# Kernel optimization log

Hardware: AMD Instinct MI355X
Metric: run time of the kernel (lower is better)

Reference implementation:

```python
import jax, jax.numpy as jnp
import numpy as np

EPS = 1e-15
BALL_EPS = 1e-5  # geoopt-style clamp away from the ball boundary


def expmap0(u):
    # Poincare ball (curvature -1): expmap0(u) = tanh(||u||) * u / ||u||
    n = jnp.linalg.norm(u, axis=-1, keepdims=True)
    n = jnp.maximum(n, EPS)
    return jnp.tanh(n) * u / n


def setup_inputs() -> dict:
    key = jax.random.key(0)
    k1, k2, k3 = jax.random.split(key, 3)
    B, H, D, L = 32768, 768, 384, 128
    cls_output = jax.random.normal(k1, (B, H), dtype=jnp.float32)
    W_proj = jax.random.normal(k2, (H, D), dtype=jnp.float32) * 0.02
    b_proj = jnp.zeros((D,), dtype=jnp.float32)
    # class prototypes: uniform(-0.1, 0.1) then expmap0, as in __init__
    tangent = jax.random.uniform(k3, (L, D), dtype=jnp.float32, minval=-0.1, maxval=0.1)
    poincare_weight = expmap0(tangent)
    return {"cls_output": cls_output, "W_proj": W_proj, "b_proj": b_proj,
            "poincare_weight": poincare_weight}


def reference(cls_output, W_proj, b_proj, poincare_weight):
    # projection (dropout is identity in eval mode)
    projected = cls_output @ W_proj + b_proj            # [B, D]
    x = expmap0(projected)                              # [B, D] points in ball
    y = poincare_weight                                 # [L, D] class reps in ball
    # Poincare distance for all (B, L) pairs, fused via dot products:
    # ||(-x) mobius+ y||^2 = ||x - y||^2 / (1 - 2<x,y> + ||x||^2 ||y||^2)
    x2 = jnp.sum(x * x, axis=-1)                        # [B]
    y2 = jnp.sum(y * y, axis=-1)                        # [L]
    xy = x @ y.T                                        # [B, L]
    sq_diff = x2[:, None] + y2[None, :] - 2.0 * xy      # ||x - y||^2
    denom = 1.0 - 2.0 * xy + x2[:, None] * y2[None, :]
    ratio = jnp.clip(sq_diff / denom, 0.0, (1.0 - BALL_EPS) ** 2)
    dist = 2.0 * jnp.arctanh(jnp.sqrt(ratio))           # [B, L]
    logits = -dist
    return logits, x
```

## Files before the change

kernel.cpp:

```cpp
#include <hip/hip_runtime.h>

typedef __attribute__((ext_vector_type(8))) short bf16x8;
typedef __attribute__((ext_vector_type(16))) float f32x16;

__device__ __forceinline__ unsigned short f2b(float f) {
  unsigned x = __builtin_bit_cast(unsigned, f);
  x += 0x7fffu + ((x >> 16) & 1u);
  return (unsigned short)(x >> 16);
}

__global__ __launch_bounds__(256) void k_prep(const float* __restrict__ W,
                                              const float* __restrict__ Y,
                                              unsigned short* __restrict__ Wt,
                                              unsigned short* __restrict__ Ybf,
                                              float* __restrict__ y2) {
  __shared__ unsigned short sT[64][72];
  int b = blockIdx.x;
  if (b < 72) {
    int bk = (b % 12) * 64, bn = (b / 12) * 64;
    int c = threadIdx.x & 63, rr = threadIdx.x >> 6;
#pragma unroll
    for (int i = 0; i < 16; i++) {
      int row = rr * 16 + i;
      sT[row][c] = f2b(W[(size_t)(bk + row) * 384 + bn + c]);
    }
    __syncthreads();
#pragma unroll
    for (int i = 0; i < 16; i++) {
      int row = rr * 16 + i;
      Wt[(size_t)(bn + row) * 768 + bk + c] = sT[c][row];
    }
  } else {
    int t = threadIdx.x;
    for (int i = t; i < 12288; i += 256) {
      float4 v = ((const float4*)Y)[i];
      ushort4 o;
      o.x = f2b(v.x); o.y = f2b(v.y); o.z = f2b(v.z); o.w = f2b(v.w);
      ((ushort4*)Ybf)[i] = o;
    }
    if (t < 128) {
      const float4* row = (const float4*)(Y + (size_t)t * 384);
      float s = 0.f;
#pragma unroll
      for (int j = 0; j < 96; j++) {
        float4 v = row[j];
        s += v.x * v.x + v.y * v.y + v.z * v.z + v.w * v.w;
      }
      y2[t] = s;
    }
  }
}

#define LDS1 72

__global__ __launch_bounds__(512, 2) void k_proj(const float* __restrict__ cls,
                                                 const unsigned short* __restrict__ Wt,
                                                 const float* __restrict__ bias,
                                                 float* __restrict__ xout,
                                                 float* __restrict__ x2out) {
  __shared__ unsigned short sA[128 * LDS1];
  __shared__ unsigned short sW[384 * LDS1];
  __shared__ float rs[128][4];
  __shared__ float sF[128];

  const int tid = threadIdx.x;
  const int bm = blockIdx.x * 128;
  const int wave = tid >> 6, lane = tid & 63;
  const int r = lane & 31, h = lane >> 5;
  const int rg = wave & 1, cg = wave >> 1;

  f32x16 acc[2][3];
#pragma unroll
  for (int i = 0; i < 2; i++)
#pragma unroll
    for (int j = 0; j < 3; j++)
#pragma unroll
      for (int e = 0; e < 16; e++) acc[i][j][e] = 0.f;

  for (int k0 = 0; k0 < 768; k0 += 64) {
    __syncthreads();
#pragma unroll
    for (int c = tid; c < 1024; c += 512) {
      int row = c >> 3, kc = c & 7;
      const float* src = cls + (size_t)(bm + row) * 768 + k0 + kc * 8;
      float4 f0 = *(const float4*)(src);
      float4 f1 = *(const float4*)(src + 4);
      uint4 p;
      p.x = (unsigned)f2b(f0.x) | ((unsigned)f2b(f0.y) << 16);
      p.y = (unsigned)f2b(f0.z) | ((unsigned)f2b(f0.w) << 16);
      p.z = (unsigned)f2b(f1.x) | ((unsigned)f2b(f1.y) << 16);
      p.w = (unsigned)f2b(f1.z) | ((unsigned)f2b(f1.w) << 16);
      *(uint4*)(sA + row * LDS1 + kc * 8) = p;
    }
#pragma unroll
    for (int c = tid; c < 3072; c += 512) {
      int row = c >> 3, kc = c & 7;
      *(uint4*)(sW + row * LDS1 + kc * 8) =
          *(const uint4*)(Wt + (size_t)row * 768 + k0 + kc * 8);
    }
    __syncthreads();
#pragma unroll
    for (int sub = 0; sub < 4; sub++) {
      const int kk = sub * 16 + h * 8;
      bf16x8 a0 = *(const bf16x8*)(sA + (rg * 64 + r) * LDS1 + kk);
      bf16x8 a1 = *(const bf16x8*)(sA + (rg * 64 + 32 + r) * LDS1 + kk);
      bf16x8 b0 = *(const bf16x8*)(sW + (cg * 96 + r) * LDS1 + kk);
      bf16x8 b1 = *(const bf16x8*)(sW + (cg * 96 + 32 + r) * LDS1 + kk);
      bf16x8 b2 = *(const bf16x8*)(sW + (cg * 96 + 64 + r) * LDS1 + kk);
      acc[0][0] = __builtin_amdgcn_mfma_f32_32x32x16_bf16(a0, b0, acc[0][0], 0, 0, 0);
      acc[0][1] = __builtin_amdgcn_mfma_f32_32x32x16_bf16(a0, b1, acc[0][1], 0, 0, 0);
      acc[0][2] = __builtin_amdgcn_mfma_f32_32x32x16_bf16(a0, b2, acc[0][2], 0, 0, 0);
      acc[1][0] = __builtin_amdgcn_mfma_f32_32x32x16_bf16(a1, b0, acc[1][0], 0, 0, 0);
      acc[1][1] = __builtin_amdgcn_mfma_f32_32x32x16_bf16(a1, b1, acc[1][1], 0, 0, 0);
      acc[1][2] = __builtin_amdgcn_mfma_f32_32x32x16_bf16(a1, b2, acc[1][2], 0, 0, 0);
    }
  }

  float bcol[3];
#pragma unroll
  for (int j = 0; j < 3; j++) bcol[j] = bias[cg * 96 + j * 32 + r];

#pragma unroll
  for (int i = 0; i < 2; i++) {
#pragma unroll
    for (int reg = 0; reg < 16; reg++) {
      float s = 0.f;
#pragma unroll
      for (int j = 0; j < 3; j++) {
        float v = acc[i][j][reg] + bcol[j];
        acc[i][j][reg] = v;
        s += v * v;
      }
      s += __shfl_xor(s, 1);
      s += __shfl_xor(s, 2);
      s += __shfl_xor(s, 4);
      s += __shfl_xor(s, 8);
      s += __shfl_xor(s, 16);
      if (r == 0) {
        int rowl = rg * 64 + i * 32 + (reg & 3) + 8 * (reg >> 2) + 4 * h;
        rs[rowl][cg] = s;
      }
    }
  }
  __syncthreads();
  if (tid < 128) {
    float n2 = rs[tid][0] + rs[tid][1] + rs[tid][2] + rs[tid][3];
    float n = fmaxf(sqrtf(n2), 1e-15f);
    float f = tanhf(n) / n;
    sF[tid] = f;
    x2out[bm + tid] = n2 * f * f;
  }
  __syncthreads();
#pragma unroll
  for (int i = 0; i < 2; i++) {
#pragma unroll
    for (int reg = 0; reg < 16; reg++) {
      int rowl = rg * 64 + i * 32 + (reg & 3) + 8 * (reg >> 2) + 4 * h;
      float f = sF[rowl];
#pragma unroll
      for (int j = 0; j < 3; j++) {
        xout[(size_t)(bm + rowl) * 384 + cg * 96 + j * 32 + r] = acc[i][j][reg] * f;
      }
    }
  }
}

#define LDS2 136

__global__ __launch_bounds__(512, 4) void k_logits(const float* __restrict__ X,
                                                   const float* __restrict__ x2,
                                                   const unsigned short* __restrict__ Y,
                                                   const float* __restrict__ y2,
                                                   float* __restrict__ out) {
  __shared__ unsigned short sX[128 * LDS2];
  __shared__ unsigned short sY[128 * LDS2];
  const int tid = threadIdx.x;
  const int bm = blockIdx.x * 128;
  const int wave = tid >> 6, lane = tid & 63;
  const int r = lane & 31, h = lane >> 5;
  const int rt = 32 * (wave & 3), ct = 64 * (wave >> 2);

  f32x16 acc[2];
#pragma unroll
  for (int j = 0; j < 2; j++)
#pragma unroll
    for (int e = 0; e < 16; e++) acc[j][e] = 0.f;

  for (int k0 = 0; k0 < 384; k0 += 128) {
    __syncthreads();
#pragma unroll
    for (int c = tid; c < 2048; c += 512) {
      int row = c >> 4, kc = c & 15;
      const float* src = X + (size_t)(bm + row) * 384 + k0 + kc * 8;
      float4 f0 = *(const float4*)(src);
      float4 f1 = *(const float4*)(src + 4);
      uint4 p;
      p.x = (unsigned)f2b(f0.x) | ((unsigned)f2b(f0.y) << 16);
      p.y = (unsigned)f2b(f0.z) | ((unsigned)f2b(f0.w) << 16);
      p.z = (unsigned)f2b(f1.x) | ((unsigned)f2b(f1.y) << 16);
      p.w = (unsigned)f2b(f1.z) | ((unsigned)f2b(f1.w) << 16);
      *(uint4*)(sX + row * LDS2 + kc * 8) = p;
    }
#pragma unroll
    for (int c = tid; c < 2048; c += 512) {
      int row = c >> 4, kc = c & 15;
      *(uint4*)(sY + row * LDS2 + kc * 8) =
          *(const uint4*)(Y + (size_t)row * 384 + k0 + kc * 8);
    }
    __syncthreads();
#pragma unroll
    for (int sub = 0; sub < 8; sub++) {
      const int kk = sub * 16 + h * 8;
      bf16x8 a = *(const bf16x8*)(sX + (rt + r) * LDS2 + kk);
      bf16x8 b0 = *(const bf16x8*)(sY + (ct + r) * LDS2 + kk);
      bf16x8 b1 = *(const bf16x8*)(sY + (ct + 32 + r) * LDS2 + kk);
      acc[0] = __builtin_amdgcn_mfma_f32_32x32x16_bf16(a, b0, acc[0], 0, 0, 0);
      acc[1] = __builtin_amdgcn_mfma_f32_32x32x16_bf16(a, b1, acc[1], 0, 0, 0);
    }
  }

  const float CLIP = 0.9999800001f;
  float yc[2] = {y2[ct + r], y2[ct + 32 + r]};
#pragma unroll
  for (int reg = 0; reg < 16; reg++) {
    int rowl = rt + (reg & 3) + 8 * (reg >> 2) + 4 * h;
    float xr = x2[bm + rowl];
#pragma unroll
    for (int j = 0; j < 2; j++) {
      float xy = acc[j][reg];
      float sq = xr + yc[j] - 2.f * xy;
      float den = 1.f - 2.f * xy + xr * yc[j];
      float ratio = fminf(fmaxf(sq / den, 0.f), CLIP);
      float s = sqrtf(ratio);
      float dist = logf((1.f + s) / (1.f - s));
      out[(size_t)(bm + rowl) * 128 + ct + j * 32 + r] = -dist;
    }
  }
}

extern "C" void kernel_launch(void* const* d_in, const int* in_sizes, int n_in,
                              void* d_out, int out_size, void* d_ws, size_t ws_size,
                              hipStream_t stream) {
  const float* cls  = (const float*)d_in[0];
  const float* W    = (const float*)d_in[1];
  const float* bias = (const float*)d_in[2];
  const float* Y    = (const float*)d_in[3];

  float* out_logits = (float*)d_out;
  float* out_x = out_logits + (size_t)32768 * 128;

  float* x2 = (float*)d_ws;
  float* y2 = x2 + 32768;
  unsigned short* Wt = (unsigned short*)(y2 + 128);
  unsigned short* Ybf = Wt + (size_t)384 * 768;

  k_prep<<<73, 256, 0, stream>>>(W, Y, Wt, Ybf, y2);
  k_proj<<<256, 512, 0, stream>>>(cls, Wt, bias, out_x, x2);
  k_logits<<<256, 512, 0, stream>>>(out_x, x2, Ybf, y2, out_logits);
}
```

Measured before the change: 233.4 us.

## Halve row tiles, prefetch next K-slice into registers, and parallelize Y prep

Both GEMM kernels now use 64-row tiles, which doubles the grid to 512 blocks and raises the k_proj occupancy hint. The next K-slice of A and W/Y is loaded into registers while MFMAs run on the current slice, so global-load latency overlaps compute. The Y bf16 conversion and y2 norms are split over 8 blocks instead of one. The trade is a higher ratio of W/Y reloads per output row and more register pressure from the prefetch buffers.

Result: slower. 285.1 us (+22.1%).

```diff
diff --git a/kernel.cpp b/kernel.cpp
--- a/kernel.cpp
+++ b/kernel.cpp
@@ -31,88 +31,106 @@
       Wt[(size_t)(bn + row) * 768 + bk + c] = sT[c][row];
     }
   } else {
+    int yb = b - 72;
     int t = threadIdx.x;
-    for (int i = t; i < 12288; i += 256) {
-      float4 v = ((const float4*)Y)[i];
+#pragma unroll
+    for (int i = 0; i < 6; i++) {
+      int idx = yb * 1536 + i * 256 + t;
+      float4 v = ((const float4*)Y)[idx];
       ushort4 o;
       o.x = f2b(v.x); o.y = f2b(v.y); o.z = f2b(v.z); o.w = f2b(v.w);
-      ((ushort4*)Ybf)[i] = o;
+      ((ushort4*)Ybf)[idx] = o;
     }
     if (t < 128) {
-      const float4* row = (const float4*)(Y + (size_t)t * 384);
+      int row = yb * 16 + (t >> 3), j = t & 7;
+      const float4* rp = (const float4*)(Y + (size_t)row * 384);
       float s = 0.f;
 #pragma unroll
-      for (int j = 0; j < 96; j++) {
-        float4 v = row[j];
+      for (int i = 0; i < 12; i++) {
+        float4 v = rp[j + i * 8];
         s += v.x * v.x + v.y * v.y + v.z * v.z + v.w * v.w;
       }
-      y2[t] = s;
+      s += __shfl_xor(s, 1);
+      s += __shfl_xor(s, 2);
+      s += __shfl_xor(s, 4);
+      if (j == 0) y2[row] = s;
     }
   }
 }
 
 #define LDS1 72
 
-__global__ __launch_bounds__(512, 2) void k_proj(const float* __restrict__ cls,
+__global__ __launch_bounds__(512, 4) void k_proj(const float* __restrict__ cls,
                                                  const unsigned short* __restrict__ Wt,
                                                  const float* __restrict__ bias,
                                                  float* __restrict__ xout,
                                                  float* __restrict__ x2out) {
-  __shared__ unsigned short sA[128 * LDS1];
+  __shared__ unsigned short sA[64 * LDS1];
   __shared__ unsigned short sW[384 * LDS1];
-  __shared__ float rs[128][4];
-  __shared__ float sF[128];
+  __shared__ float rs[64][4];
+  __shared__ float sF[64];
 
   const int tid = threadIdx.x;
-  const int bm = blockIdx.x * 128;
+  const int bm = blockIdx.x * 64;
   const int wave = tid >> 6, lane = tid & 63;
   const int r = lane & 31, h = lane >> 5;
   const int rg = wave & 1, cg = wave >> 1;
 
-  f32x16 acc[2][3];
-#pragma unroll
-  for (int i = 0; i < 2; i++)
-#pragma unroll
-    for (int j = 0; j < 3; j++)
-#pragma unroll
-      for (int e = 0; e < 16; e++) acc[i][j][e] = 0.f;
+  const int arow = tid >> 3, akc = tid & 7;
+  const float* aptr = cls + (size_t)(bm + arow) * 768 + akc * 8;
+  const unsigned short* asd = sA + arow * LDS1 + akc * 8;
+
+  f32x16 acc[3];
+#pragma unroll
+  for (int j = 0; j < 3; j++)
+#pragma unroll
+    for (int e = 0; e < 16; e++) acc[j][e] = 0.f;
+
+  uint4 wv[6];
+  float4 af0, af1;
+
+#pragma unroll
+  for (int i = 0; i < 6; i++) {
+    int c = tid + i * 512, row = c >> 3, kc = c & 7;
+    wv[i] = *(const uint4*)(Wt + (size_t)row * 768 + kc * 8);
+  }
+  af0 = *(const float4*)(aptr);
+  af1 = *(const float4*)(aptr + 4);
 
   for (int k0 = 0; k0 < 768; k0 += 64) {
     __syncthreads();
-#pragma unroll
-    for (int c = tid; c < 1024; c += 512) {
-      int row = c >> 3, kc = c & 7;
-      const float* src = cls + (size_t)(bm + row) * 768 + k0 + kc * 8;
-      float4 f0 = *(const float4*)(src);
-      float4 f1 = *(const float4*)(src + 4);
-      uint4 p;
-      p.x = (unsigned)f2b(f0.x) | ((unsigned)f2b(f0.y) << 16);
-      p.y = (unsigned)f2b(f0.z) | ((unsigned)f2b(f0.w) << 16);
-      p.z = (unsigned)f2b(f1.x) | ((unsigned)f2b(f1.y) << 16);
-      p.w = (unsigned)f2b(f1.z) | ((unsigned)f2b(f1.w) << 16);
-      *(uint4*)(sA + row * LDS1 + kc * 8) = p;
-    }
-#pragma unroll
-    for (int c = tid; c < 3072; c += 512) {
-      int row = c >> 3, kc = c & 7;
-      *(uint4*)(sW + row * LDS1 + kc * 8) =
-          *(const uint4*)(Wt + (size_t)row * 768 + k0 + kc * 8);
-    }
-    __syncthreads();
+    uint4 ap;
+    ap.x = (unsigned)f2b(af0.x) | ((unsigned)f2b(af0.y) << 16);
+    ap.y = (unsigned)f2b(af0.z) | ((unsigned)f2b(af0.w) << 16);
+    ap.z = (unsigned)f2b(af1.x) | ((unsigned)f2b(af1.y) << 16);
+    ap.w = (unsigned)f2b(af1.z) | ((unsigned)f2b(af1.w) << 16);
+    *(uint4*)asd = ap;
+#pragma unroll
+    for (int i = 0; i < 6; i++) {
+      int c = tid + i * 512, row = c >> 3, kc = c & 7;
+      *(uint4*)(sW + row * LDS1 + kc * 8) = wv[i];
+    }
+    __syncthreads();
+    if (k0 + 64 < 768) {
+      int kn = k0 + 64;
+#pragma unroll
+      for (int i = 0; i < 6; i++) {
+        int c = tid + i * 512, row = c >> 3, kc = c & 7;
+        wv[i] = *(const uint4*)(Wt + (size_t)row * 768 + kn + kc * 8);
+      }
+      af0 = *(const float4*)(aptr + kn);
+      af1 = *(const float4*)(aptr + kn + 4);
+    }
 #pragma unroll
     for (int sub = 0; sub < 4; sub++) {
       const int kk = sub * 16 + h * 8;
-      bf16x8 a0 = *(const bf16x8*)(sA + (rg * 64 + r) * LDS1 + kk);
-      bf16x8 a1 = *(const bf16x8*)(sA + (rg * 64 + 32 + r) * LDS1 + kk);
+      bf16x8 a = *(const bf16x8*)(sA + (rg * 32 + r) * LDS1 + kk);
       bf16x8 b0 = *(const bf16x8*)(sW + (cg * 96 + r) * LDS1 + kk);
       bf16x8 b1 = *(const bf16x8*)(sW + (cg * 96 + 32 + r) * LDS1 + kk);
       bf16x8 b2 = *(const bf16x8*)(sW + (cg * 96 + 64 + r) * LDS1 + kk);
-      acc[0][0] = __builtin_amdgcn_mfma_f32_32x32x16_bf16(a0, b0, acc[0][0], 0, 0, 0);
-      acc[0][1] = __builtin_amdgcn_mfma_f32_32x32x16_bf16(a0, b1, acc[0][1], 0, 0, 0);
-      acc[0][2] = __builtin_amdgcn_mfma_f32_32x32x16_bf16(a0, b2, acc[0][2], 0, 0, 0);
-      acc[1][0] = __builtin_amdgcn_mfma_f32_32x32x16_bf16(a1, b0, acc[1][0], 0, 0, 0);
-      acc[1][1] = __builtin_amdgcn_mfma_f32_32x32x16_bf16(a1, b1, acc[1][1], 0, 0, 0);
-      acc[1][2] = __builtin_amdgcn_mfma_f32_32x32x16_bf16(a1, b2, acc[1][2], 0, 0, 0);
+      acc[0] = __builtin_amdgcn_mfma_f32_32x32x16_bf16(a, b0, acc[0], 0, 0, 0);
+      acc[1] = __builtin_amdgcn_mfma_f32_32x32x16_bf16(a, b1, acc[1], 0, 0, 0);
+      acc[2] = __builtin_amdgcn_mfma_f32_32x32x16_bf16(a, b2, acc[2], 0, 0, 0);
     }
   }
 
@@ -121,29 +139,26 @@
   for (int j = 0; j < 3; j++) bcol[j] = bias[cg * 96 + j * 32 + r];
 
 #pragma unroll
-  for (int i = 0; i < 2; i++) {
-#pragma unroll
-    for (int reg = 0; reg < 16; reg++) {
-      float s = 0.f;
-#pragma unroll
-      for (int j = 0; j < 3; j++) {
-        float v = acc[i][j][reg] + bcol[j];
-        acc[i][j][reg] = v;
-        s += v * v;
-      }
-      s += __shfl_xor(s, 1);
-      s += __shfl_xor(s, 2);
-      s += __shfl_xor(s, 4);
-      s += __shfl_xor(s, 8);
-      s += __shfl_xor(s, 16);
-      if (r == 0) {
-        int rowl = rg * 64 + i * 32 + (reg & 3) + 8 * (reg >> 2) + 4 * h;
-        rs[rowl][cg] = s;
-      }
+  for (int reg = 0; reg < 16; reg++) {
+    float s = 0.f;
+#pragma unroll
+    for (int j = 0; j < 3; j++) {
+      float v = acc[j][reg] + bcol[j];
+      acc[j][reg] = v;
+      s += v * v;
+    }
+    s += __shfl_xor(s, 1);
+    s += __shfl_xor(s, 2);
+    s += __shfl_xor(s, 4);
+    s += __shfl_xor(s, 8);
+    s += __shfl_xor(s, 16);
+    if (r == 0) {
+      int rowl = rg * 32 + (reg & 3) + 8 * (reg >> 2) + 4 * h;
+      rs[rowl][cg] = s;
     }
   }
   __syncthreads();
-  if (tid < 128) {
+  if (tid < 64) {
     float n2 = rs[tid][0] + rs[tid][1] + rs[tid][2] + rs[tid][3];
     float n = fmaxf(sqrtf(n2), 1e-15f);
     float f = tanhf(n) / n;
@@ -152,15 +167,12 @@
   }
   __syncthreads();
 #pragma unroll
-  for (int i = 0; i < 2; i++) {
-#pragma unroll
-    for (int reg = 0; reg < 16; reg++) {
-      int rowl = rg * 64 + i * 32 + (reg & 3) + 8 * (reg >> 2) + 4 * h;
-      float f = sF[rowl];
-#pragma unroll
-      for (int j = 0; j < 3; j++) {
-        xout[(size_t)(bm + rowl) * 384 + cg * 96 + j * 32 + r] = acc[i][j][reg] * f;
-      }
+  for (int reg = 0; reg < 16; reg++) {
+    int rowl = rg * 32 + (reg & 3) + 8 * (reg >> 2) + 4 * h;
+    float f = sF[rowl];
+#pragma unroll
+    for (int j = 0; j < 3; j++) {
+      xout[(size_t)(bm + rowl) * 384 + cg * 96 + j * 32 + r] = acc[j][reg] * f;
     }
   }
 }
@@ -172,69 +184,83 @@
                                                    const unsigned short* __restrict__ Y,
                                                    const float* __restrict__ y2,
                                                    float* __restrict__ out) {
-  __shared__ unsigned short sX[128 * LDS2];
+  __shared__ unsigned short sX[64 * LDS2];
   __shared__ unsigned short sY[128 * LDS2];
   const int tid = threadIdx.x;
-  const int bm = blockIdx.x * 128;
+  const int bm = blockIdx.x * 64;
   const int wave = tid >> 6, lane = tid & 63;
   const int r = lane & 31, h = lane >> 5;
-  const int rt = 32 * (wave & 3), ct = 64 * (wave >> 2);
-
-  f32x16 acc[2];
-#pragma unroll
-  for (int j = 0; j < 2; j++)
-#pragma unroll
-    for (int e = 0; e < 16; e++) acc[j][e] = 0.f;
+  const int rt = 32 * (wave & 1), ct = 32 * (wave >> 1);
+
+  const int xrow = tid >> 3, xkc = tid & 7;
+  const float* xptr = X + (size_t)(bm + xrow) * 384 + xkc * 16;
+
+  f32x16 acc;
+#pragma unroll
+  for (int e = 0; e < 16; e++) acc[e] = 0.f;
+
+  float4 xf[4];
+  uint4 yv[4];
+
+#pragma unroll
+  for (int i = 0; i < 4; i++) xf[i] = *(const float4*)(xptr + i * 4);
+#pragma unroll
+  for (int i = 0; i < 4; i++) {
+    int c = tid + i * 512, row = c >> 4, kc = c & 15;
+    yv[i] = *(const uint4*)(Y + (size_t)row * 384 + kc * 8);
+  }
 
   for (int k0 = 0; k0 < 384; k0 += 128) {
     __syncthreads();
-#pragma unroll
-    for (int c = tid; c < 2048; c += 512) {
-      int row = c >> 4, kc = c & 15;
-      const float* src = X + (size_t)(bm + row) * 384 + k0 + kc * 8;
-      float4 f0 = *(const float4*)(src);
-      float4 f1 = *(const float4*)(src + 4);
-      uint4 p;
-      p.x = (unsigned)f2b(f0.x) | ((unsigned)f2b(f0.y) << 16);
-      p.y = (unsigned)f2b(f0.z) | ((unsigned)f2b(f0.w) << 16);
-      p.z = (unsigned)f2b(f1.x) | ((unsigned)f2b(f1.y) << 16);
-      p.w = (unsigned)f2b(f1.z) | ((unsigned)f2b(f1.w) << 16);
-      *(uint4*)(sX + row * LDS2 + kc * 8) = p;
-    }
-#pragma unroll
-    for (int c = tid; c < 2048; c += 512) {
-      int row = c >> 4, kc = c & 15;
-      *(uint4*)(sY + row * LDS2 + kc * 8) =
-          *(const uint4*)(Y + (size_t)row * 384 + k0 + kc * 8);
-    }
-    __syncthreads();
+    uint4 p0, p1;
+    p0.x = (unsigned)f2b(xf[0].x) | ((unsigned)f2b(xf[0].y) << 16);
+    p0.y = (unsigned)f2b(xf[0].z) | ((unsigned)f2b(xf[0].w) << 16);
+    p0.z = (unsigned)f2b(xf[1].x) | ((unsigned)f2b(xf[1].y) << 16);
+    p0.w = (unsigned)f2b(xf[1].z) | ((unsigned)f2b(xf[1].w) << 16);
+    p1.x = (unsigned)f2b(xf[2].x) | ((unsigned)f2b(xf[2].y) << 16);
+    p1.y = (unsigned)f2b(xf[2].z) | ((unsigned)f2b(xf[2].w) << 16);
+    p1.z = (unsigned)f2b(xf[3].x) | ((unsigned)f2b(xf[3].y) << 16);
+    p1.w = (unsigned)f2b(xf[3].z) | ((unsigned)f2b(xf[3].w) << 16);
+    *(uint4*)(sX + xrow * LDS2 + xkc * 16) = p0;
+    *(uint4*)(sX + xrow * LDS2 + xkc * 16 + 8) = p1;
+#pragma unroll
+    for (int i = 0; i < 4; i++) {
+      int c = tid + i * 512, row = c >> 4, kc = c & 15;
+      *(uint4*)(sY + row * LDS2 + kc * 8) = yv[i];
+    }
+    __syncthreads();
+    if (k0 + 128 < 384) {
+      int kn = k0 + 128;
+#pragma unroll
+      for (int i = 0; i < 4; i++) xf[i] = *(const float4*)(xptr + kn + i * 4);
+#pragma unroll
+      for (int i = 0; i < 4; i++) {
+        int c = tid + i * 512, row = c >> 4, kc = c & 15;
+        yv[i] = *(const uint4*)(Y + (size_t)row * 384 + kn + kc * 8);
+      }
+    }
 #pragma unroll
     for (int sub = 0; sub < 8; sub++) {
       const int kk = sub * 16 + h * 8;
       bf16x8 a = *(const bf16x8*)(sX + (rt + r) * LDS2 + kk);
-      bf16x8 b0 = *(const bf16x8*)(sY + (ct + r) * LDS2 + kk);
-      bf16x8 b1 = *(const bf16x8*)(sY + (ct + 32 + r) * LDS2 + kk);
-      acc[0] = __builtin_amdgcn_mfma_f32_32x32x16_bf16(a, b0, acc[0], 0, 0, 0);
-      acc[1] = __builtin_amdgcn_mfma_f32_32x32x16_bf16(a, b1, acc[1], 0, 0, 0);
+      bf16x8 b = *(const bf16x8*)(sY + (ct + r) * LDS2 + kk);
+      acc = __builtin_amdgcn_mfma_f32_32x32x16_bf16(a, b, acc, 0, 0, 0);
     }
   }
 
   const float CLIP = 0.9999800001f;
-  float yc[2] = {y2[ct + r], y2[ct + 32 + r]};
+  float yc = y2[ct + r];
 #pragma unroll
   for (int reg = 0; reg < 16; reg++) {
     int rowl = rt + (reg & 3) + 8 * (reg >> 2) + 4 * h;
     float xr = x2[bm + rowl];
-#pragma unroll
-    for (int j = 0; j < 2; j++) {
-      float xy = acc[j][reg];
-      float sq = xr + yc[j] - 2.f * xy;
-      float den = 1.f - 2.f * xy + xr * yc[j];
-      float ratio = fminf(fmaxf(sq / den, 0.f), CLIP);
-      float s = sqrtf(ratio);
-      float dist = logf((1.f + s) / (1.f - s));
-      out[(size_t)(bm + rowl) * 128 + ct + j * 32 + r] = -dist;
-    }
+    float xy = acc[reg];
+    float sq = xr + yc - 2.f * xy;
+    float den = 1.f - 2.f * xy + xr * yc;
+    float ratio = fminf(fmaxf(sq / den, 0.f), CLIP);
+    float s = sqrtf(ratio);
+    float dist = logf((1.f + s) / (1.f - s));
+    out[(size_t)(bm + rowl) * 128 + ct + r] = -dist;
   }
 }
 
@@ -254,7 +280,7 @@
   unsigned short* Wt = (unsigned short*)(y2 + 128);
   unsigned short* Ybf = Wt + (size_t)384 * 768;
 
-  k_prep<<<73, 256, 0, stream>>>(W, Y, Wt, Ybf, y2);
-  k_proj<<<256, 512, 0, stream>>>(cls, Wt, bias, out_x, x2);
-  k_logits<<<256, 512, 0, stream>>>(out_x, x2, Ybf, y2, out_logits);
-}
+  k_prep<<<80, 256, 0, stream>>>(W, Y, Wt, Ybf, y2);
+  k_proj<<<512, 512, 0, stream>>>(cls, Wt, bias, out_x, x2);
+  k_logits<<<512, 512, 0, stream>>>(out_x, x2, Ybf, y2, out_logits);
+}
```
